# Optimization experiments

Hardware: AMD Instinct MI355X
Metric: run time of the kernel (lower is better)

## Reference

```python
import jax, jax.numpy as jnp
import numpy as np

B, S, D = 16, 2048, 128
NEG = -1e9


def setup_inputs() -> dict:
    key = jax.random.key(0)
    kq, kk, kv = jax.random.split(key, 3)
    queries = jax.random.normal(kq, (B, S, D), dtype=jnp.float32)
    keys = jax.random.normal(kk, (B, S, D), dtype=jnp.float32)
    values = jax.random.normal(kv, (B, S, D), dtype=jnp.float32)
    # causal additive mask: 0 on/below diagonal, -1e9 above
    causal = jnp.triu(jnp.ones((S, S), dtype=jnp.float32), k=1) * NEG
    return {"queries": queries, "keys": keys, "values": values, "mask": causal}


def reference(queries, keys, values, mask):
    d = queries.shape[-1]
    scale = 1.0 / jnp.sqrt(jnp.asarray(d, dtype=queries.dtype))
    # scores: [b, q, k]
    scores = jnp.einsum("bqd,bkd->bqk", queries, keys) * scale
    scores = scores + mask  # broadcast [S,S] over batch
    weights = jax.nn.softmax(scores, axis=-1)
    # dropout p=0.0 in eval mode -> identity
    return jnp.einsum("bqk,bkd->bqd", weights, values)
```

## Files before the change

### kernel.cpp

```cpp
#include <hip/hip_runtime.h>
#include <hip/hip_bf16.h>
#include <cstdint>

#define SS   2048
#define DD   128
#define KBLK 64
#define NKT  32
#define TILE_BYTES 16384

#define NBLK 1152
#define WS_K    ((size_t)0)
#define WS_V    ((size_t)16 * NKT * TILE_BYTES)
#define WS_PO   ((size_t)16 * NKT * TILE_BYTES * 2)
#define WS_ML   (WS_PO + (size_t)NBLK * 128 * 128 * 2)
#define WS_NEED (WS_ML + (size_t)NBLK * 128 * 4)

typedef __attribute__((ext_vector_type(8)))  short short8;
typedef __attribute__((ext_vector_type(16))) float f32x16;
typedef __attribute__((ext_vector_type(4)))  float f32x4;

__device__ __forceinline__ unsigned short f2bf(float x) {
  return __builtin_bit_cast(unsigned short, (__bf16)x);
}
__device__ __forceinline__ float bfbits2f(unsigned int lo16shifted) {
  return __builtin_bit_cast(float, lo16shifted);
}

__device__ __constant__ unsigned char SLOT_BASE[16] = {0,1,2,4,6,9,12,16,20,25,30,36,42,49,56,64};
__device__ __constant__ unsigned char NCH[16]       = {1,1,2,2,3,3,4,4,5,5,6,6,7,7,8,8};
__device__ __constant__ unsigned char SLOT_I[72] = {
  0,1,2,2,3,3,4,4,4,5,5,5,6,6,6,6,7,7,7,7,
  8,8,8,8,8,9,9,9,9,9,10,10,10,10,10,10,11,11,11,11,11,11,
  12,12,12,12,12,12,12,13,13,13,13,13,13,13,
  14,14,14,14,14,14,14,14,15,15,15,15,15,15,15,15};

__global__ __launch_bounds__(256) void prepack_kv8(
    const float* __restrict__ K, const float* __restrict__ V, char* __restrict__ ws)
{
  __shared__ float st[64][132];
  const int b = blockIdx.x, t = blockIdx.y;
  const int tid = threadIdx.x;
  const float* Kt = K + ((size_t)b * SS + t * KBLK) * DD;
  const float* Vt = V + ((size_t)b * SS + t * KBLK) * DD;
  char* Kd = ws + WS_K + ((size_t)(b * NKT + t)) * TILE_BYTES;
  char* Vd = ws + WS_V + ((size_t)(b * NKT + t)) * TILE_BYTES;

  #pragma unroll
  for (int u = 0; u < 4; ++u) {
    int row = u * 16 + (tid >> 4);
    int col = 8 * (tid & 15);
    const float4* sp = reinterpret_cast<const float4*>(Kt + (size_t)row * DD + col);
    float4 x = sp[0], y = sp[1];
    *reinterpret_cast<float4*>(&st[row][col])     = x;
    *reinterpret_cast<float4*>(&st[row][col + 4]) = y;
  }
  __syncthreads();
  #pragma unroll
  for (int u = 0; u < 4; ++u) {
    int e = u * 256 + tid;
    int g = e >> 9, s = (e >> 6) & 7, lane = e & 63;
    int h = lane >> 5, l31 = lane & 31;
    int key = g * 32 + l31;
    int d0 = s * 16 + h * 8;
    float4 x = *reinterpret_cast<const float4*>(&st[key][d0]);
    float4 y = *reinterpret_cast<const float4*>(&st[key][d0 + 4]);
    short8 w;
    w[0] = f2bf(x.x); w[1] = f2bf(x.y); w[2] = f2bf(x.z); w[3] = f2bf(x.w);
    w[4] = f2bf(y.x); w[5] = f2bf(y.y); w[6] = f2bf(y.z); w[7] = f2bf(y.w);
    *reinterpret_cast<short8*>(Kd + e * 16) = w;
  }
  __syncthreads();

  #pragma unroll
  for (int u = 0; u < 4; ++u) {
    int row = u * 16 + (tid >> 4);
    int col = 8 * (tid & 15);
    const float4* sp = reinterpret_cast<const float4*>(Vt + (size_t)row * DD + col);
    float4 x = sp[0], y = sp[1];
    *reinterpret_cast<float4*>(&st[row][col])     = x;
    *reinterpret_cast<float4*>(&st[row][col + 4]) = y;
  }
  __syncthreads();
  #pragma unroll
  for (int u = 0; u < 4; ++u) {
    int e = u * 256 + tid;
    int dg = e >> 8, s4 = (e >> 6) & 3, lane = e & 63;
    int h = lane >> 5, l31 = lane & 31;
    int d = dg * 32 + l31;
    int y8 = s4 * 2 + h;
    short8 w;
    #pragma unroll
    for (int j = 0; j < 8; ++j) {
      int a = ((y8 >> 2) << 5) | (((y8 >> 1) & 1) << 4) | ((j >> 2) << 3) | (j & 3) | ((y8 & 1) << 2);
      w[j] = f2bf(st[a][d]);
    }
    *reinterpret_cast<short8*>(Vd + e * 16) = w;
  }
}

__global__ __launch_bounds__(256) void sdpa_v8(
    const float* __restrict__ Q, const char* __restrict__ ws,
    float* __restrict__ O, unsigned short* __restrict__ partO,
    float* __restrict__ partML)
{
  const int y = blockIdx.x;
  const int b = y & 15;
  const int slot = y >> 4;
  const int i = SLOT_I[slot];
  const int c = slot - SLOT_BASE[i];
  const int nch = NCH[i];
  const int ntile = (c == nch - 1) ? (2 * i + 2 - 4 * c) : 4;
  const int kvt0 = 4 * c;
  const bool dostore = (nch == 1);

  const int tid  = threadIdx.x;
  const int lane = tid & 63;
  const int wid  = tid >> 6;
  const int l31  = lane & 31;
  const int h    = lane >> 5;

  const float* Qb  = Q + (size_t)b * SS * DD;
  const char*  Kws = ws + WS_K + ((size_t)(b * NKT)) * TILE_BYTES;
  const char*  Vws = ws + WS_V + ((size_t)(b * NKT)) * TILE_BYTES;

  const float qscale = 0.08838834764831845f * 1.4426950408889634f;
  const int qg = 128 * i + wid * 32 + l31;

  short8 qf[8];
  {
    const float* qrow = Qb + (size_t)qg * DD;
    #pragma unroll
    for (int s = 0; s < 8; ++s) {
      const float4* p = reinterpret_cast<const float4*>(qrow + s * 16 + h * 8);
      float4 x = p[0], z = p[1];
      short8 w;
      w[0] = f2bf(x.x * qscale); w[1] = f2bf(x.y * qscale);
      w[2] = f2bf(x.z * qscale); w[3] = f2bf(x.w * qscale);
      w[4] = f2bf(z.x * qscale); w[5] = f2bf(z.y * qscale);
      w[6] = f2bf(z.z * qscale); w[7] = f2bf(z.w * qscale);
      qf[s] = w;
    }
  }

  f32x16 o[4];
  #pragma unroll
  for (int dg = 0; dg < 4; ++dg)
    #pragma unroll
    for (int r = 0; r < 16; ++r) o[dg][r] = 0.f;
  float lsum = 0.f;

  for (int t = 0; t < ntile; ++t) {
    const int tt = kvt0 + t;
    const char* Kt = Kws + (size_t)tt * TILE_BYTES;
    const char* Vt = Vws + (size_t)tt * TILE_BYTES;
    const bool domask = tt >= 2 * i;

    short8 pf[4];
    float psum = 0.f;

    #pragma unroll
    for (int g = 0; g < 2; ++g) {
      short8 kf[8];
      #pragma unroll
      for (int s = 0; s < 8; ++s)
        kf[s] = *reinterpret_cast<const short8*>(Kt + g * 8192 + s * 1024 + lane * 16);

      f32x16 acc;
      #pragma unroll
      for (int r = 0; r < 16; ++r) acc[r] = 0.f;
      __builtin_amdgcn_s_setprio(1);
      #pragma unroll
      for (int s = 0; s < 8; ++s)
        acc = __builtin_amdgcn_mfma_f32_32x32x16_bf16(kf[s], qf[s], acc, 0, 0, 0);
      __builtin_amdgcn_s_setprio(0);

      if (domask) {
        const int kb = tt * 64 + g * 32 + 4 * h;
        #pragma unroll
        for (int r = 0; r < 16; ++r) {
          int keyg = kb + (r & 3) + 8 * (r >> 2);
          if (keyg > qg) acc[r] = -1e30f;
        }
      }

      float pg[16];
      #pragma unroll
      for (int r = 0; r < 16; ++r) pg[r] = exp2f(acc[r]);
      float s0 = ((pg[0]+pg[1])+(pg[2]+pg[3])) + ((pg[4]+pg[5])+(pg[6]+pg[7]));
      float s1 = ((pg[8]+pg[9])+(pg[10]+pg[11])) + ((pg[12]+pg[13])+(pg[14]+pg[15]));
      psum += s0 + s1;

      short8 w0, w1;
      #pragma unroll
      for (int j = 0; j < 8; ++j) { w0[j] = f2bf(pg[j]); w1[j] = f2bf(pg[8 + j]); }
      pf[2 * g]     = w0;
      pf[2 * g + 1] = w1;
    }
    lsum += psum;

    #pragma unroll
    for (int dg = 0; dg < 4; ++dg) {
      short8 vf[4];
      #pragma unroll
      for (int s4 = 0; s4 < 4; ++s4)
        vf[s4] = *reinterpret_cast<const short8*>(Vt + (dg * 4 + s4) * 1024 + lane * 16);
      __builtin_amdgcn_s_setprio(1);
      #pragma unroll
      for (int s4 = 0; s4 < 4; ++s4)
        o[dg] = __builtin_amdgcn_mfma_f32_32x32x16_bf16(vf[s4], pf[s4], o[dg], 0, 0, 0);
      __builtin_amdgcn_s_setprio(0);
    }
  }

  lsum += __shfl_xor(lsum, 32);

  if (dostore) {
    float inv = 1.0f / lsum;
    float* Ob = O + (size_t)b * SS * DD + (size_t)qg * DD;
    #pragma unroll
    for (int dg = 0; dg < 4; ++dg)
      #pragma unroll
      for (int rq = 0; rq < 4; ++rq) {
        int d0 = dg * 32 + 8 * rq + 4 * h;
        float4 w;
        w.x = o[dg][4 * rq + 0] * inv;
        w.y = o[dg][4 * rq + 1] * inv;
        w.z = o[dg][4 * rq + 2] * inv;
        w.w = o[dg][4 * rq + 3] * inv;
        *reinterpret_cast<float4*>(Ob + d0) = w;
      }
  } else {
    unsigned short* po = partO + (size_t)y * (128 * 128) + (size_t)(wid * 32 + l31) * 128;
    #pragma unroll
    for (int dg = 0; dg < 4; ++dg)
      #pragma unroll
      for (int rq = 0; rq < 4; ++rq) {
        int d0 = dg * 32 + 8 * rq + 4 * h;
        ushort4 u;
        u.x = f2bf(o[dg][4 * rq + 0]);
        u.y = f2bf(o[dg][4 * rq + 1]);
        u.z = f2bf(o[dg][4 * rq + 2]);
        u.w = f2bf(o[dg][4 * rq + 3]);
        *reinterpret_cast<ushort4*>(po + d0) = u;
      }
    if (h == 0) partML[y * 128 + wid * 32 + l31] = lsum;
  }
}

__global__ __launch_bounds__(256) void merge_v8(
    const unsigned short* __restrict__ partO, const float* __restrict__ partML,
    float* __restrict__ O)
{
  const int b = blockIdx.x;
  const int i = blockIdx.y + 2;
  const int rg = blockIdx.z;
  const int tid = threadIdx.x;
  const int row = rg * 32 + (tid >> 3);
  const int c0  = (tid & 7) * 16;

  float acc[16];
  #pragma unroll
  for (int u = 0; u < 16; ++u) acc[u] = 0.f;
  float ltot = 0.f;

  const int nch = NCH[i];
  const int base = SLOT_BASE[i];

  for (int c = 0; c < nch; ++c) {
    int slot = (base + c) * 16 + b;
    ltot += partML[slot * 128 + row];
    const uint4* po = reinterpret_cast<const uint4*>(
        partO + (size_t)slot * (128 * 128) + (size_t)row * 128 + c0);
    #pragma unroll
    for (int u = 0; u < 2; ++u) {
      uint4 v = po[u];
      acc[u*8+0] += bfbits2f(v.x << 16); acc[u*8+1] += bfbits2f(v.x & 0xffff0000u);
      acc[u*8+2] += bfbits2f(v.y << 16); acc[u*8+3] += bfbits2f(v.y & 0xffff0000u);
      acc[u*8+4] += bfbits2f(v.z << 16); acc[u*8+5] += bfbits2f(v.z & 0xffff0000u);
      acc[u*8+6] += bfbits2f(v.w << 16); acc[u*8+7] += bfbits2f(v.w & 0xffff0000u);
    }
  }
  float inv = 1.0f / ltot;
  float* orow = O + ((size_t)b * SS + 128 * i + row) * DD + c0;
  #pragma unroll
  for (int u = 0; u < 4; ++u) {
    float4 w;
    w.x = acc[4*u+0] * inv; w.y = acc[4*u+1] * inv;
    w.z = acc[4*u+2] * inv; w.w = acc[4*u+3] * inv;
    reinterpret_cast<float4*>(orow)[u] = w;
  }
}

__device__ __forceinline__ int sigma_col(int a) {
  return (a & 35) | ((a & 12) << 1) | ((a & 16) >> 2);
}

__global__ __launch_bounds__(256) void sdpa_naive(
    const float* __restrict__ Q, const float* __restrict__ K,
    const float* __restrict__ V, float* __restrict__ O)
{
  __shared__ __align__(16) char smem[64 * 128 * 2 * 2];
  char* Klds  = smem;
  char* Vtlds = smem + 64 * 128 * 2;

  const int b   = blockIdx.x;
  const int qb  = (int)gridDim.y - 1 - (int)blockIdx.y;
  const int q0  = qb * 64;
  const int tid = threadIdx.x;
  const int lane = tid & 63;
  const int wid  = tid >> 6;
  const int l15  = lane & 15;
  const int hi   = lane >> 4;

  const float* Qb = Q + (size_t)b * SS * DD;
  const float* Kb = K + (size_t)b * SS * DD;
  const float* Vb = V + (size_t)b * SS * DD;
  float*       Ob = O + (size_t)b * SS * DD;
  const float scale = 0.08838834764831845f;

  short8 qf[4];
  {
    const float* qrow = Qb + (size_t)(q0 + wid * 16 + l15) * DD;
    #pragma unroll
    for (int cc = 0; cc < 4; ++cc) {
      const float4* p = reinterpret_cast<const float4*>(qrow + 32 * cc + 8 * hi);
      float4 x = p[0], yv = p[1];
      short8 w;
      w[0]=f2bf(x.x*scale); w[1]=f2bf(x.y*scale); w[2]=f2bf(x.z*scale); w[3]=f2bf(x.w*scale);
      w[4]=f2bf(yv.x*scale); w[5]=f2bf(yv.y*scale); w[6]=f2bf(yv.z*scale); w[7]=f2bf(yv.w*scale);
      qf[cc] = w;
    }
  }

  f32x4 o[8];
  #pragma unroll
  for (int nt = 0; nt < 8; ++nt) o[nt] = (f32x4){0.f,0.f,0.f,0.f};
  float m = -INFINITY, lsum = 0.f;

  const int ntile = qb + 1;
  for (int t = 0; t < ntile; ++t) {
    const int kv0 = t * 64;
    if (t) __syncthreads();
    #pragma unroll
    for (int u = 0; u < 4; ++u) {
      int row = u * 16 + (tid >> 4);
      int col = 8 * (tid & 15);
      const float4* sp = reinterpret_cast<const float4*>(Kb + (size_t)(kv0 + row) * DD + col);
      float4 x = sp[0], yv = sp[1];
      short8 w;
      w[0]=f2bf(x.x); w[1]=f2bf(x.y); w[2]=f2bf(x.z); w[3]=f2bf(x.w);
      w[4]=f2bf(yv.x); w[5]=f2bf(yv.y); w[6]=f2bf(yv.z); w[7]=f2bf(yv.w);
      int off = (row * 256 + col * 2) ^ ((row & 7) << 4);
      *reinterpret_cast<short8*>(Klds + off) = w;
    }
    #pragma unroll
    for (int u = 0; u < 4; ++u) {
      int row = u * 16 + (tid >> 4);
      int col = 8 * (tid & 15);
      const float4* sp = reinterpret_cast<const float4*>(Vb + (size_t)(kv0 + row) * DD + col);
      float4 x = sp[0], yv = sp[1];
      int sc = sigma_col(row);
      float vals[8] = {x.x, x.y, x.z, x.w, yv.x, yv.y, yv.z, yv.w};
      #pragma unroll
      for (int j = 0; j < 8; ++j) {
        int d = col + j;
        int off = ((d << 7) + (sc << 1)) ^ ((((d >> 3) ^ d) & 7) << 4);
        *reinterpret_cast<unsigned short*>(Vtlds + off) = f2bf(vals[j]);
      }
    }
    __syncthreads();

    f32x4 sacc[4];
    #pragma unroll
    for (int g = 0; g < 4; ++g) {
      f32x4 acc = {0.f,0.f,0.f,0.f};
      #pragma unroll
      for (int cc = 0; cc < 4; ++cc) {
        int row = g * 16 + l15;
        int off = (row * 256 + (32 * cc + 8 * hi) * 2) ^ ((row & 7) << 4);
        short8 kf = *reinterpret_cast<const short8*>(Klds + off);
        acc = __builtin_amdgcn_mfma_f32_16x16x32_bf16(kf, qf[cc], acc, 0, 0, 0);
      }
      sacc[g] = acc;
    }
    if (t == ntile - 1) {
      const int q = q0 + wid * 16 + l15;
      #pragma unroll
      for (int g = 0; g < 4; ++g)
        #pragma unroll
        for (int ii = 0; ii < 4; ++ii) {
          int key = kv0 + g * 16 + 4 * hi + ii;
          if (key > q) sacc[g][ii] = -1e30f;
        }
    }
    float tmax = -INFINITY;
    #pragma unroll
    for (int g = 0; g < 4; ++g)
      #pragma unroll
      for (int ii = 0; ii < 4; ++ii) tmax = fmaxf(tmax, sacc[g][ii]);
    tmax = fmaxf(tmax, __shfl_xor(tmax, 16));
    tmax = fmaxf(tmax, __shfl_xor(tmax, 32));
    float mnew = fmaxf(m, tmax);
    float corr = __expf(m - mnew);
    m = mnew;
    float p[4][4]; float psum = 0.f;
    #pragma unroll
    for (int g = 0; g < 4; ++g)
      #pragma unroll
      for (int ii = 0; ii < 4; ++ii) {
        float pv = __expf(sacc[g][ii] - mnew);
        p[g][ii] = pv; psum += pv;
      }
    psum += __shfl_xor(psum, 16);
    psum += __shfl_xor(psum, 32);
    lsum = lsum * corr + psum;
    float corrO[4];
    #pragma unroll
    for (int ii = 0; ii < 4; ++ii) corrO[ii] = __shfl(corr, 4 * hi + ii);
    #pragma unroll
    for (int nt = 0; nt < 8; ++nt)
      #pragma unroll
      for (int ii = 0; ii < 4; ++ii) o[nt][ii] *= corrO[ii];
    short8 pfr[2];
    #pragma unroll
    for (int ks = 0; ks < 2; ++ks) {
      short8 w;
      #pragma unroll
      for (int ii = 0; ii < 4; ++ii) { w[ii] = f2bf(p[2*ks][ii]); w[4+ii] = f2bf(p[2*ks+1][ii]); }
      pfr[ks] = w;
    }
    #pragma unroll
    for (int ks = 0; ks < 2; ++ks)
      #pragma unroll
      for (int nt = 0; nt < 8; ++nt) {
        int d = nt * 16 + l15;
        int off = ((d << 7) + (ks * 32 + 8 * hi) * 2) ^ ((((d >> 3) ^ d) & 7) << 4);
        short8 vvf = *reinterpret_cast<const short8*>(Vtlds + off);
        o[nt] = __builtin_amdgcn_mfma_f32_16x16x32_bf16(pfr[ks], vvf, o[nt], 0, 0, 0);
      }
  }
  float rl = 1.0f / lsum;
  float rlO[4];
  #pragma unroll
  for (int ii = 0; ii < 4; ++ii) rlO[ii] = __shfl(rl, 4 * hi + ii);
  const int qrow = q0 + wid * 16;
  #pragma unroll
  for (int nt = 0; nt < 8; ++nt)
    #pragma unroll
    for (int ii = 0; ii < 4; ++ii)
      Ob[(size_t)(qrow + 4 * hi + ii) * DD + nt * 16 + l15] = o[nt][ii] * rlO[ii];
}

extern "C" void kernel_launch(void* const* d_in, const int* in_sizes, int n_in,
                              void* d_out, int out_size, void* d_ws, size_t ws_size,
                              hipStream_t stream) {
  const float* Q = (const float*)d_in[0];
  const float* K = (const float*)d_in[1];
  const float* V = (const float*)d_in[2];
  float* O = (float*)d_out;
  char* ws = (char*)d_ws;

  if (ws_size >= WS_NEED) {
    unsigned short* partO = (unsigned short*)(ws + WS_PO);
    float* partML = (float*)(ws + WS_ML);
    prepack_kv8<<<dim3(16, NKT), 256, 0, stream>>>(K, V, ws);
    sdpa_v8<<<dim3(NBLK), 256, 0, stream>>>(Q, ws, O, partO, partML);
    merge_v8<<<dim3(16, 14, 4), 256, 0, stream>>>(partO, partML, O);
  } else {
    sdpa_naive<<<dim3(16, 32), 256, 0, stream>>>(Q, K, V, O);
  }
}
```

Measured before the change: 71.22 us.

## Stage K/V tiles through LDS with register prefetch and halve split-KV chunk count

The attention kernel now has each wave copy a quarter of the current K/V tile from global memory into shared memory. The next tile is prefetched into registers while the current one is consumed, so all four waves share one global load per tile instead of each reading it separately. KV chunks per block grow from 4 to 8 tiles, cutting the block count from 1152 to 640 and reducing the partial outputs the merge kernel must combine. The cost is two barriers per tile, 32KB of LDS per block that may limit occupancy, and longer-running blocks with fewer of them to fill the GPU.

```diff
diff --git a/kernel.cpp b/kernel.cpp
--- a/kernel.cpp
+++ b/kernel.cpp
@@ -8,7 +8,7 @@
 #define NKT  32
 #define TILE_BYTES 16384
 
-#define NBLK 1152
+#define NBLK 640
 #define WS_K    ((size_t)0)
 #define WS_V    ((size_t)16 * NKT * TILE_BYTES)
 #define WS_PO   ((size_t)16 * NKT * TILE_BYTES * 2)
@@ -26,15 +26,13 @@
   return __builtin_bit_cast(float, lo16shifted);
 }
 
-__device__ __constant__ unsigned char SLOT_BASE[16] = {0,1,2,4,6,9,12,16,20,25,30,36,42,49,56,64};
-__device__ __constant__ unsigned char NCH[16]       = {1,1,2,2,3,3,4,4,5,5,6,6,7,7,8,8};
-__device__ __constant__ unsigned char SLOT_I[72] = {
-  0,1,2,2,3,3,4,4,4,5,5,5,6,6,6,6,7,7,7,7,
-  8,8,8,8,8,9,9,9,9,9,10,10,10,10,10,10,11,11,11,11,11,11,
-  12,12,12,12,12,12,12,13,13,13,13,13,13,13,
-  14,14,14,14,14,14,14,14,15,15,15,15,15,15,15,15};
-
-__global__ __launch_bounds__(256) void prepack_kv8(
+__device__ __constant__ unsigned char V10_I[40] = {
+  0,1,2,3, 4,4,5,5,6,6,7,7, 8,8,8,9,9,9,10,10,10,11,11,11,
+  12,12,12,12,13,13,13,13,14,14,14,14,15,15,15,15};
+__device__ __constant__ unsigned char V10_BASE[16] = {0,1,2,3,4,6,8,10,12,15,18,21,24,28,32,36};
+__device__ __constant__ unsigned char V10_NCH[16]  = {1,1,1,1,2,2,2,2,3,3,3,3,4,4,4,4};
+
+__global__ __launch_bounds__(256) void prepack_kv10(
     const float* __restrict__ K, const float* __restrict__ V, char* __restrict__ ws)
 {
   __shared__ float st[64][132];
@@ -98,19 +96,22 @@
   }
 }
 
-__global__ __launch_bounds__(256) void sdpa_v8(
+__global__ __launch_bounds__(256) void sdpa_v10(
     const float* __restrict__ Q, const char* __restrict__ ws,
     float* __restrict__ O, unsigned short* __restrict__ partO,
     float* __restrict__ partML)
 {
+  __shared__ __align__(16) char smem[32768];
+
   const int y = blockIdx.x;
   const int b = y & 15;
   const int slot = y >> 4;
-  const int i = SLOT_I[slot];
-  const int c = slot - SLOT_BASE[i];
-  const int nch = NCH[i];
-  const int ntile = (c == nch - 1) ? (2 * i + 2 - 4 * c) : 4;
-  const int kvt0 = 4 * c;
+  const int i = V10_I[slot];
+  const int c = slot - V10_BASE[i];
+  const int nch = V10_NCH[i];
+  const int tiles = 2 * i + 2;
+  const int kvt0 = 8 * c;
+  const int ntile = (tiles - kvt0 < 8) ? (tiles - kvt0) : 8;
   const bool dostore = (nch == 1);
 
   const int tid  = threadIdx.x;
@@ -142,6 +143,27 @@
     }
   }
 
+  const char* gsrc = (wid < 2) ? (Kws + wid * 8192) : (Vws + (wid - 2) * 8192);
+  char* ldst = (wid < 2) ? (smem + wid * 8192) : (smem + 16384 + (wid - 2) * 8192);
+
+  uint4 rs[8];
+  {
+    const char* src = gsrc + (size_t)kvt0 * TILE_BYTES;
+    #pragma unroll
+    for (int j = 0; j < 8; ++j)
+      rs[j] = *reinterpret_cast<const uint4*>(src + j * 1024 + lane * 16);
+  }
+  #pragma unroll
+  for (int j = 0; j < 8; ++j)
+    *reinterpret_cast<uint4*>(ldst + j * 1024 + lane * 16) = rs[j];
+  __syncthreads();
+  if (ntile > 1) {
+    const char* src = gsrc + (size_t)(kvt0 + 1) * TILE_BYTES;
+    #pragma unroll
+    for (int j = 0; j < 8; ++j)
+      rs[j] = *reinterpret_cast<const uint4*>(src + j * 1024 + lane * 16);
+  }
+
   f32x16 o[4];
   #pragma unroll
   for (int dg = 0; dg < 4; ++dg)
@@ -151,8 +173,6 @@
 
   for (int t = 0; t < ntile; ++t) {
     const int tt = kvt0 + t;
-    const char* Kt = Kws + (size_t)tt * TILE_BYTES;
-    const char* Vt = Vws + (size_t)tt * TILE_BYTES;
     const bool domask = tt >= 2 * i;
 
     short8 pf[4];
@@ -163,7 +183,7 @@
       short8 kf[8];
       #pragma unroll
       for (int s = 0; s < 8; ++s)
-        kf[s] = *reinterpret_cast<const short8*>(Kt + g * 8192 + s * 1024 + lane * 16);
+        kf[s] = *reinterpret_cast<const short8*>(smem + g * 8192 + s * 1024 + lane * 16);
 
       f32x16 acc;
       #pragma unroll
@@ -198,17 +218,31 @@
     }
     lsum += psum;
 
+    __builtin_amdgcn_s_setprio(1);
     #pragma unroll
     for (int dg = 0; dg < 4; ++dg) {
       short8 vf[4];
       #pragma unroll
       for (int s4 = 0; s4 < 4; ++s4)
-        vf[s4] = *reinterpret_cast<const short8*>(Vt + (dg * 4 + s4) * 1024 + lane * 16);
-      __builtin_amdgcn_s_setprio(1);
+        vf[s4] = *reinterpret_cast<const short8*>(smem + 16384 + (dg * 4 + s4) * 1024 + lane * 16);
       #pragma unroll
       for (int s4 = 0; s4 < 4; ++s4)
         o[dg] = __builtin_amdgcn_mfma_f32_32x32x16_bf16(vf[s4], pf[s4], o[dg], 0, 0, 0);
-      __builtin_amdgcn_s_setprio(0);
+    }
+    __builtin_amdgcn_s_setprio(0);
+
+    __syncthreads();
+    if (t + 1 < ntile) {
+      #pragma unroll
+      for (int j = 0; j < 8; ++j)
+        *reinterpret_cast<uint4*>(ldst + j * 1024 + lane * 16) = rs[j];
+      if (t + 2 < ntile) {
+        const char* src = gsrc + (size_t)(kvt0 + t + 2) * TILE_BYTES;
+        #pragma unroll
+        for (int j = 0; j < 8; ++j)
+          rs[j] = *reinterpret_cast<const uint4*>(src + j * 1024 + lane * 16);
+      }
+      __syncthreads();
     }
   }
 
@@ -247,12 +281,12 @@
   }
 }
 
-__global__ __launch_bounds__(256) void merge_v8(
+__global__ __launch_bounds__(256) void merge_v10(
     const unsigned short* __restrict__ partO, const float* __restrict__ partML,
     float* __restrict__ O)
 {
   const int b = blockIdx.x;
-  const int i = blockIdx.y + 2;
+  const int i = blockIdx.y + 4;
   const int rg = blockIdx.z;
   const int tid = threadIdx.x;
   const int row = rg * 32 + (tid >> 3);
@@ -263,8 +297,8 @@
   for (int u = 0; u < 16; ++u) acc[u] = 0.f;
   float ltot = 0.f;
 
-  const int nch = NCH[i];
-  const int base = SLOT_BASE[i];
+  const int nch = V10_NCH[i];
+  const int base = V10_BASE[i];
 
   for (int c = 0; c < nch; ++c) {
     int slot = (base + c) * 16 + b;
@@ -463,9 +497,9 @@
   if (ws_size >= WS_NEED) {
     unsigned short* partO = (unsigned short*)(ws + WS_PO);
     float* partML = (float*)(ws + WS_ML);
-    prepack_kv8<<<dim3(16, NKT), 256, 0, stream>>>(K, V, ws);
-    sdpa_v8<<<dim3(NBLK), 256, 0, stream>>>(Q, ws, O, partO, partML);
-    merge_v8<<<dim3(16, 14, 4), 256, 0, stream>>>(partO, partML, O);
+    prepack_kv10<<<dim3(16, NKT), 256, 0, stream>>>(K, V, ws);
+    sdpa_v10<<<dim3(NBLK), 256, 0, stream>>>(Q, ws, O, partO, partML);
+    merge_v10<<<dim3(16, 12, 4), 256, 0, stream>>>(partO, partML, O);
   } else {
     sdpa_naive<<<dim3(16, 32), 256, 0, stream>>>(Q, K, V, O);
   }
```

Measured after the change: 95.90 us. 34.7% more time.

## Use 256-row query blocks with double-buffered LDS staging of K/V tiles

Applied to the files above, without the earlier changes.

Each workgroup now has 8 waves (512 threads) covering 256 query rows, and K/V tiles are processed in 128-key periods. Each pair of tiles is staged into LDS with global_load_lds and double-buffered so the next pair loads while the current one is computed. Every K/V tile fetched from global memory is shared across more query rows, which cuts global/L2 traffic and lets loads overlap compute. In exchange, the grid shrinks from 1152 to 320 blocks, 128 KB of LDS per block limits occupancy, and the split/merge tables and partial buffers are resized to match.

```diff
diff --git a/kernel.cpp b/kernel.cpp
--- a/kernel.cpp
+++ b/kernel.cpp
@@ -8,12 +8,12 @@
 #define NKT  32
 #define TILE_BYTES 16384
 
-#define NBLK 1152
+#define NBLK11 320
 #define WS_K    ((size_t)0)
 #define WS_V    ((size_t)16 * NKT * TILE_BYTES)
 #define WS_PO   ((size_t)16 * NKT * TILE_BYTES * 2)
-#define WS_ML   (WS_PO + (size_t)NBLK * 128 * 128 * 2)
-#define WS_NEED (WS_ML + (size_t)NBLK * 128 * 4)
+#define WS_ML   (WS_PO + (size_t)NBLK11 * 256 * 128 * 2)
+#define WS_NEED (WS_ML + (size_t)NBLK11 * 256 * 4)
 
 typedef __attribute__((ext_vector_type(8)))  short short8;
 typedef __attribute__((ext_vector_type(16))) float f32x16;
@@ -26,15 +26,11 @@
   return __builtin_bit_cast(float, lo16shifted);
 }
 
-__device__ __constant__ unsigned char SLOT_BASE[16] = {0,1,2,4,6,9,12,16,20,25,30,36,42,49,56,64};
-__device__ __constant__ unsigned char NCH[16]       = {1,1,2,2,3,3,4,4,5,5,6,6,7,7,8,8};
-__device__ __constant__ unsigned char SLOT_I[72] = {
-  0,1,2,2,3,3,4,4,4,5,5,5,6,6,6,6,7,7,7,7,
-  8,8,8,8,8,9,9,9,9,9,10,10,10,10,10,10,11,11,11,11,11,11,
-  12,12,12,12,12,12,12,13,13,13,13,13,13,13,
-  14,14,14,14,14,14,14,14,15,15,15,15,15,15,15,15};
-
-__global__ __launch_bounds__(256) void prepack_kv8(
+__device__ __constant__ unsigned char V11_I[20]    = {0,1,2,2,3,3,4,4,4,5,5,5,6,6,6,6,7,7,7,7};
+__device__ __constant__ unsigned char V11_BASE[8]  = {0,1,2,4,6,9,12,16};
+__device__ __constant__ unsigned char V11_NCH[8]   = {1,1,2,2,3,3,4,4};
+
+__global__ __launch_bounds__(256) void prepack_kv11(
     const float* __restrict__ K, const float* __restrict__ V, char* __restrict__ ws)
 {
   __shared__ float st[64][132];
@@ -98,19 +94,43 @@
   }
 }
 
-__global__ __launch_bounds__(256) void sdpa_v8(
+__device__ __forceinline__ void stage_pair(const char* Kws, const char* Vws, int p,
+                                           char* Kl, char* Vl, int wid, int lane)
+{
+  const char* Ksrc = Kws + (size_t)(2 * p) * TILE_BYTES;
+  const char* Vsrc = Vws + (size_t)(2 * p) * TILE_BYTES;
+  #pragma unroll
+  for (int j = 0; j < 4; ++j) {
+    int off = j * 8192 + wid * 1024;
+    __builtin_amdgcn_global_load_lds(
+        (const __attribute__((address_space(1))) unsigned int*)(Ksrc + off + lane * 16),
+        (__attribute__((address_space(3))) unsigned int*)(Kl + off), 16, 0, 0);
+  }
+  #pragma unroll
+  for (int j = 0; j < 4; ++j) {
+    int off = j * 8192 + wid * 1024;
+    __builtin_amdgcn_global_load_lds(
+        (const __attribute__((address_space(1))) unsigned int*)(Vsrc + off + lane * 16),
+        (__attribute__((address_space(3))) unsigned int*)(Vl + off), 16, 0, 0);
+  }
+}
+
+__global__ __launch_bounds__(512) void sdpa_v11(
     const float* __restrict__ Q, const char* __restrict__ ws,
     float* __restrict__ O, unsigned short* __restrict__ partO,
     float* __restrict__ partML)
 {
+  __shared__ __align__(16) char smem[2 * 65536];
+
   const int y = blockIdx.x;
   const int b = y & 15;
   const int slot = y >> 4;
-  const int i = SLOT_I[slot];
-  const int c = slot - SLOT_BASE[i];
-  const int nch = NCH[i];
-  const int ntile = (c == nch - 1) ? (2 * i + 2 - 4 * c) : 4;
-  const int kvt0 = 4 * c;
+  const int i = V11_I[slot];
+  const int c = slot - V11_BASE[i];
+  const int nch = V11_NCH[i];
+  const int periods = 2 * i + 2;
+  const int p0 = 4 * c;
+  const int ntile = (periods - p0 < 4) ? (periods - p0) : 4;
   const bool dostore = (nch == 1);
 
   const int tid  = threadIdx.x;
@@ -124,7 +144,7 @@
   const char*  Vws = ws + WS_V + ((size_t)(b * NKT)) * TILE_BYTES;
 
   const float qscale = 0.08838834764831845f * 1.4426950408889634f;
-  const int qg = 128 * i + wid * 32 + l31;
+  const int qg = 256 * i + wid * 32 + l31;
 
   short8 qf[8];
   {
@@ -149,21 +169,30 @@
     for (int r = 0; r < 16; ++r) o[dg][r] = 0.f;
   float lsum = 0.f;
 
+  int cur = 0;
+  stage_pair(Kws, Vws, p0, smem, smem + 32768, wid, lane);
+  __syncthreads();
+
   for (int t = 0; t < ntile; ++t) {
-    const int tt = kvt0 + t;
-    const char* Kt = Kws + (size_t)tt * TILE_BYTES;
-    const char* Vt = Vws + (size_t)tt * TILE_BYTES;
-    const bool domask = tt >= 2 * i;
-
-    short8 pf[4];
+    const int p = p0 + t;
+    if (t + 1 < ntile) {
+      char* nb = smem + (cur ^ 1) * 65536;
+      stage_pair(Kws, Vws, p + 1, nb, nb + 32768, wid, lane);
+    }
+    const char* Kl = smem + cur * 65536;
+    const char* Vl = Kl + 32768;
+    const bool domask = (p >= 2 * i);
+
+    short8 pf[8];
     float psum = 0.f;
 
     #pragma unroll
-    for (int g = 0; g < 2; ++g) {
+    for (int g = 0; g < 4; ++g) {
+      const char* Kg = Kl + (g >> 1) * 16384 + (g & 1) * 8192;
       short8 kf[8];
       #pragma unroll
       for (int s = 0; s < 8; ++s)
-        kf[s] = *reinterpret_cast<const short8*>(Kt + g * 8192 + s * 1024 + lane * 16);
+        kf[s] = *reinterpret_cast<const short8*>(Kg + s * 1024 + lane * 16);
 
       f32x16 acc;
       #pragma unroll
@@ -175,7 +204,7 @@
       __builtin_amdgcn_s_setprio(0);
 
       if (domask) {
-        const int kb = tt * 64 + g * 32 + 4 * h;
+        const int kb = p * 128 + g * 32 + 4 * h;
         #pragma unroll
         for (int r = 0; r < 16; ++r) {
           int keyg = kb + (r & 3) + 8 * (r >> 2);
@@ -198,17 +227,21 @@
     }
     lsum += psum;
 
+    __builtin_amdgcn_s_setprio(1);
     #pragma unroll
     for (int dg = 0; dg < 4; ++dg) {
-      short8 vf[4];
-      #pragma unroll
-      for (int s4 = 0; s4 < 4; ++s4)
-        vf[s4] = *reinterpret_cast<const short8*>(Vt + (dg * 4 + s4) * 1024 + lane * 16);
-      __builtin_amdgcn_s_setprio(1);
-      #pragma unroll
-      for (int s4 = 0; s4 < 4; ++s4)
-        o[dg] = __builtin_amdgcn_mfma_f32_32x32x16_bf16(vf[s4], pf[s4], o[dg], 0, 0, 0);
-      __builtin_amdgcn_s_setprio(0);
+      #pragma unroll
+      for (int s8 = 0; s8 < 8; ++s8) {
+        const char* Vg = Vl + (s8 >> 2) * 16384 + (dg * 4 + (s8 & 3)) * 1024;
+        short8 vf8 = *reinterpret_cast<const short8*>(Vg + lane * 16);
+        o[dg] = __builtin_amdgcn_mfma_f32_32x32x16_bf16(vf8, pf[s8], o[dg], 0, 0, 0);
+      }
+    }
+    __builtin_amdgcn_s_setprio(0);
+
+    if (t + 1 < ntile) {
+      __syncthreads();
+      cur ^= 1;
     }
   }
 
@@ -230,7 +263,7 @@
         *reinterpret_cast<float4*>(Ob + d0) = w;
       }
   } else {
-    unsigned short* po = partO + (size_t)y * (128 * 128) + (size_t)(wid * 32 + l31) * 128;
+    unsigned short* po = partO + (size_t)y * (256 * 128) + (size_t)(wid * 32 + l31) * 128;
     #pragma unroll
     for (int dg = 0; dg < 4; ++dg)
       #pragma unroll
@@ -243,11 +276,11 @@
         u.w = f2bf(o[dg][4 * rq + 3]);
         *reinterpret_cast<ushort4*>(po + d0) = u;
       }
-    if (h == 0) partML[y * 128 + wid * 32 + l31] = lsum;
-  }
-}
-
-__global__ __launch_bounds__(256) void merge_v8(
+    if (h == 0) partML[y * 256 + wid * 32 + l31] = lsum;
+  }
+}
+
+__global__ __launch_bounds__(256) void merge_v11(
     const unsigned short* __restrict__ partO, const float* __restrict__ partML,
     float* __restrict__ O)
 {
@@ -263,14 +296,14 @@
   for (int u = 0; u < 16; ++u) acc[u] = 0.f;
   float ltot = 0.f;
 
-  const int nch = NCH[i];
-  const int base = SLOT_BASE[i];
+  const int nch = V11_NCH[i];
+  const int base = V11_BASE[i];
 
   for (int c = 0; c < nch; ++c) {
     int slot = (base + c) * 16 + b;
-    ltot += partML[slot * 128 + row];
+    ltot += partML[slot * 256 + row];
     const uint4* po = reinterpret_cast<const uint4*>(
-        partO + (size_t)slot * (128 * 128) + (size_t)row * 128 + c0);
+        partO + (size_t)slot * (256 * 128) + (size_t)row * 128 + c0);
     #pragma unroll
     for (int u = 0; u < 2; ++u) {
       uint4 v = po[u];
@@ -281,7 +314,7 @@
     }
   }
   float inv = 1.0f / ltot;
-  float* orow = O + ((size_t)b * SS + 128 * i + row) * DD + c0;
+  float* orow = O + ((size_t)b * SS + 256 * i + row) * DD + c0;
   #pragma unroll
   for (int u = 0; u < 4; ++u) {
     float4 w;
@@ -463,9 +496,9 @@
   if (ws_size >= WS_NEED) {
     unsigned short* partO = (unsigned short*)(ws + WS_PO);
     float* partML = (float*)(ws + WS_ML);
-    prepack_kv8<<<dim3(16, NKT), 256, 0, stream>>>(K, V, ws);
-    sdpa_v8<<<dim3(NBLK), 256, 0, stream>>>(Q, ws, O, partO, partML);
-    merge_v8<<<dim3(16, 14, 4), 256, 0, stream>>>(partO, partML, O);
+    prepack_kv11<<<dim3(16, NKT), 256, 0, stream>>>(K, V, ws);
+    sdpa_v11<<<dim3(NBLK11), 512, 0, stream>>>(Q, ws, O, partO, partML);
+    merge_v11<<<dim3(16, 6, 8), 256, 0, stream>>>(partO, partML, O);
   } else {
     sdpa_naive<<<dim3(16, 32), 256, 0, stream>>>(Q, K, V, O);
   }
```

After: 63.18 us. 11.3% less time.
